# Kernel optimization log

Hardware: AMD Instinct MI355X
Metric: run time of the kernel (lower is better)

The kernel has to match this reference:

```python
import jax, jax.numpy as jnp
import numpy as np

C = 1024      # BIGNET_DIM
GROUPS = 256  # (1024*1024) / group_size(4096)

def _dequant(q4, norm):
    # q4: [GROUPS, 2048] ints in [0,256) packing two 4-bit codes per byte
    # (even positions = low nibble, odd positions = high nibble, as in
    #  block_quantize_4bit / block_dequantize_4bit). norm: [GROUPS, 1].
    lo = q4 % 16
    hi = q4 // 16
    q8 = jnp.stack([lo, hi], axis=-1).reshape(GROUPS, -1).astype(jnp.float32)  # [GROUPS, 4096]
    w = (q8 / 15.0 * 2.0 - 1.0) * norm
    return w.reshape(C, C)  # [out_features, in_features]

def setup_inputs() -> dict:
    key = jax.random.key(0)
    ks = jax.random.split(key, 6)
    x = jax.random.normal(ks[0], (16384, C), jnp.float32)
    wq4 = jax.random.randint(ks[1], (18, GROUPS, 2048), 0, 256, jnp.int32)
    wnorm = jax.random.uniform(ks[2], (18, GROUPS, 1), dtype=jnp.float32) * 0.05 + 1e-3
    lora_a = jax.random.normal(ks[3], (3, 32, C), jnp.float32) * 0.02
    lora_b = jax.random.normal(ks[4], (3, C, 32), jnp.float32) * 0.01
    ln_gamma = jnp.ones((5, C), jnp.float32)
    ln_beta = jnp.zeros((5, C), jnp.float32)
    return {"x": x, "wq4": wq4, "wnorm": wnorm, "lora_a": lora_a,
            "lora_b": lora_b, "ln_gamma": ln_gamma, "ln_beta": ln_beta}

def reference(x, wq4, wnorm, lora_a, lora_b, ln_gamma, ln_beta):
    def lin(h, i):
        # dequantize group-wise int4 weight, then linear (bias=False)
        return h @ _dequant(wq4[i], wnorm[i]).T

    def block(h, b, li):
        y = lin(h, 3 * b)
        if li is not None:  # QLoRALinear: parallel fp32 low-rank path
            y = y + (h @ lora_a[li].T) @ lora_b[li].T
        y = jax.nn.relu(y)
        y = jax.nn.relu(lin(y, 3 * b + 1))
        y = lin(y, 3 * b + 2)
        return y + h  # residual

    def ln(h, i):
        mu = jnp.mean(h, axis=-1, keepdims=True)
        var = jnp.mean((h - mu) ** 2, axis=-1, keepdims=True)
        return (h - mu) * jax.lax.rsqrt(var + 1e-5) * ln_gamma[i] + ln_beta[i]

    h = block(x, 0, 0); h = ln(h, 0)
    h = block(h, 1, None); h = ln(h, 1)
    h = block(h, 2, 1); h = ln(h, 2)
    h = block(h, 3, None); h = ln(h, 3)
    h = block(h, 4, 2); h = ln(h, 4)
    h = block(h, 5, None)
    return h
```

## Files before the change

### kernel.cpp

```cpp
#include <hip/hip_runtime.h>

typedef __bf16 bf16x8 __attribute__((ext_vector_type(8)));
typedef float f32x4 __attribute__((ext_vector_type(4)));

__device__ __forceinline__ unsigned short f32_to_bf16u(float f) {
  unsigned int u = __float_as_uint(f);
  u += 0x7fffu + ((u >> 16) & 1u);
  return (unsigned short)(u >> 16);
}
__device__ __forceinline__ float bf16u_to_f32(unsigned short s) {
  return __uint_as_float((unsigned int)s << 16);
}

__device__ __forceinline__ void async_copy16(const void* gptr, void* lptr) {
  __builtin_amdgcn_global_load_lds(
      (__attribute__((address_space(1))) void*)(unsigned long long)gptr,
      (__attribute__((address_space(3))) void*)(unsigned long long)lptr,
      16, 0, 0);
}

__global__ __launch_bounds__(256) void lora_ba_kernel(
    const float* __restrict__ lora_a, const float* __restrict__ lora_b,
    float* __restrict__ Wba)
{
  const int bid = blockIdx.x;
  const int li = bid >> 10;
  const int o = bid & 1023;
  const float* B = lora_b + li * 32768 + o * 32;
  const float* A = lora_a + li * 32768;
  const int c = threadIdx.x * 4;
  float4 acc = {0.f, 0.f, 0.f, 0.f};
#pragma unroll
  for (int r = 0; r < 32; r++) {
    const float br = B[r];
    const float4 a = *(const float4*)&A[r * 1024 + c];
    acc.x += br * a.x; acc.y += br * a.y; acc.z += br * a.z; acc.w += br * a.w;
  }
  *(float4*)&Wba[((size_t)li << 20) + o * 1024 + c] = acc;
}

__global__ __launch_bounds__(256) void dequant_kernel(
    const int* __restrict__ wq4, const float* __restrict__ wnorm,
    const float* __restrict__ Wba, unsigned short* __restrict__ Wd)
{
  const int gi = blockIdx.x * 256 + threadIdx.x;
  const int w = gi >> 19;
  const int rem = gi & 524287;
  const int q = wq4[gi];
  const float norm = wnorm[(w << 8) + (rem >> 11)];
  float w0 = ((float)(q & 15) * (2.0f / 15.0f) - 1.0f) * norm;
  float w1 = ((float)(q >> 4) * (2.0f / 15.0f) - 1.0f) * norm;
  const int p = rem << 1;
  const int li = (w == 0) ? 0 : (w == 6) ? 1 : (w == 12) ? 2 : -1;
  if (li >= 0) {
    const float2 ba = *(const float2*)&Wba[((size_t)li << 20) + p];
    w0 += ba.x;
    w1 += ba.y;
  }
  const unsigned int packed =
      ((unsigned int)f32_to_bf16u(w1) << 16) | (unsigned int)f32_to_bf16u(w0);
  *(unsigned int*)&Wd[((size_t)w << 20) + p] = packed;
}

__global__ __launch_bounds__(256) void cast_bf16_kernel(
    const float* __restrict__ x, unsigned short* __restrict__ o)
{
  const int i = blockIdx.x * 256 + threadIdx.x;
  const float4 v = ((const float4*)x)[i];
  ushort4 b;
  b.x = f32_to_bf16u(v.x);
  b.y = f32_to_bf16u(v.y);
  b.z = f32_to_bf16u(v.z);
  b.w = f32_to_bf16u(v.w);
  ((ushort4*)o)[i] = b;
}

template <int EPIL>
__global__ __launch_bounds__(512, 2) void gemm_bt(
    const unsigned short* __restrict__ A, const unsigned short* __restrict__ W,
    void* __restrict__ Out, const unsigned short* __restrict__ Res)
{
  constexpr int K = 1024;
  constexpr int N = 1024;
  __shared__ unsigned short lds[2][4][8192];

  const int tid = threadIdx.x;
  const int lane = tid & 63;
  const int wv = tid >> 6;
  const int wm = wv >> 2;
  const int wn = wv & 3;

  const int bid = blockIdx.x;
  const int l = (bid & 7) * 32 + (bid >> 3);
  const int m0 = (l >> 2) << 8;
  const int n0 = (l & 3) << 8;

  const int fr = lane & 15;
  const int q = lane >> 4;
  const int fr7 = fr & 7;

  const int srow = tid >> 3;
  const int schk = (tid & 7) ^ (srow & 7);
  const unsigned short* Asrc = A + (size_t)(m0 + srow) * K + schk * 8;
  const int nb0 = ((srow >> 5) << 6) + (srow & 31);
  const unsigned short* Wsrc = W + (size_t)(n0 + nb0) * K + schk * 8;

#define STAGE_A(mq, dbuf, kt)                                          \
  do {                                                                 \
    const unsigned short* s_ = Asrc + (size_t)(mq) * 64 * K + (kt);    \
    unsigned short* d_ = &lds[dbuf][(mq) ? 2 : 0][tid * 8];            \
    async_copy16(s_, d_);                                              \
    async_copy16(s_ + (size_t)128 * K, d_ + 4096);                     \
  } while (0)
#define STAGE_B(nq, dbuf, kt)                                          \
  do {                                                                 \
    const unsigned short* s_ = Wsrc + (size_t)(nq) * 32 * K + (kt);    \
    unsigned short* d_ = &lds[dbuf][(nq) ? 3 : 1][tid * 8];            \
    async_copy16(s_, d_);                                              \
    async_copy16(s_ + (size_t)128 * K, d_ + 4096);                     \
  } while (0)

  const int a_lane = (wm * 64 + fr) * 64;
  const int b_lane = (wn * 32 + fr) * 64;
  const int c0 = (q ^ fr7) << 3;
  const int c1 = ((4 + q) ^ fr7) << 3;

#define LDA4(dbuf, mq)                                                               \
  do {                                                                               \
    _Pragma("unroll") for (int ri = 0; ri < 4; ++ri) {                               \
      af[ri][0] = *(const bf16x8*)&lds[dbuf][(mq) ? 2 : 0][a_lane + ri * 1024 + c0]; \
      af[ri][1] = *(const bf16x8*)&lds[dbuf][(mq) ? 2 : 0][a_lane + ri * 1024 + c1]; \
    }                                                                                \
  } while (0)
#define LDB2(dst, dbuf, nq)                                                          \
  do {                                                                               \
    _Pragma("unroll") for (int rj = 0; rj < 2; ++rj) {                               \
      dst[rj][0] = *(const bf16x8*)&lds[dbuf][(nq) ? 3 : 1][b_lane + rj * 1024 + c0];\
      dst[rj][1] = *(const bf16x8*)&lds[dbuf][(nq) ? 3 : 1][b_lane + rj * 1024 + c1];\
    }                                                                                \
  } while (0)

#define MFMA16(ib, jb, BB)                                                    \
  do {                                                                        \
    __builtin_amdgcn_s_setprio(1);                                            \
    _Pragma("unroll") for (int i2 = 0; i2 < 4; ++i2)                          \
    _Pragma("unroll") for (int j2 = 0; j2 < 2; ++j2) {                        \
      acc[(ib) + i2][(jb) + j2] = __builtin_amdgcn_mfma_f32_16x16x32_bf16(    \
          af[i2][0], BB[j2][0], acc[(ib) + i2][(jb) + j2], 0, 0, 0);          \
      acc[(ib) + i2][(jb) + j2] = __builtin_amdgcn_mfma_f32_16x16x32_bf16(    \
          af[i2][1], BB[j2][1], acc[(ib) + i2][(jb) + j2], 0, 0, 0);          \
    }                                                                         \
    __builtin_amdgcn_s_setprio(0);                                            \
  } while (0)

#define OPEN_BAR  __builtin_amdgcn_s_barrier()
#define CLOSE_BAR asm volatile("s_barrier" ::: "memory")

  f32x4 acc[8][4];
#pragma unroll
  for (int a_ = 0; a_ < 8; ++a_)
#pragma unroll
    for (int b_ = 0; b_ < 4; ++b_) acc[a_][b_] = (f32x4){0.f, 0.f, 0.f, 0.f};

  bf16x8 af[4][2], bf0[2][2], bf1[2][2];

  STAGE_A(0, 0, 0);
  STAGE_B(0, 0, 0);
  STAGE_A(1, 0, 0);
  STAGE_B(1, 0, 0);
  STAGE_A(0, 1, 64);
  STAGE_B(0, 1, 64);
  STAGE_A(1, 1, 64);
  asm volatile("s_waitcnt vmcnt(6)" ::: "memory");
  __builtin_amdgcn_s_barrier();
  LDA4(0, 0);
  LDB2(bf0, 0, 0);

  for (int it = 0; it < K / 128; ++it) {
    const int kb = it * 128;
    const int k2 = (kb + 128 < K) ? (kb + 128) : (K - 64);
    const int k3 = (kb + 192 < K) ? (kb + 192) : (K - 64);

    LDB2(bf1, 0, 1);
    STAGE_B(1, 1, kb + 64);
    OPEN_BAR;
    MFMA16(0, 0, bf0);
    CLOSE_BAR;
    STAGE_A(0, 0, k2);
    OPEN_BAR;
    MFMA16(0, 2, bf1);
    LDA4(0, 1);
    CLOSE_BAR;
    STAGE_B(0, 0, k2);
    OPEN_BAR;
    MFMA16(4, 0, bf0);
    asm volatile("s_waitcnt vmcnt(4)" ::: "memory");
    CLOSE_BAR;
    LDB2(bf0, 1, 0);
    STAGE_A(1, 0, k2);
    OPEN_BAR;
    MFMA16(4, 2, bf1);
    LDA4(1, 0);
    CLOSE_BAR;
    LDB2(bf1, 1, 1);
    STAGE_B(1, 0, k2);
    OPEN_BAR;
    MFMA16(0, 0, bf0);
    CLOSE_BAR;
    STAGE_A(0, 1, k3);
    OPEN_BAR;
    MFMA16(0, 2, bf1);
    LDA4(1, 1);
    CLOSE_BAR;
    STAGE_B(0, 1, k3);
    OPEN_BAR;
    MFMA16(4, 0, bf0);
    asm volatile("s_waitcnt vmcnt(4)" ::: "memory");
    CLOSE_BAR;
    LDB2(bf0, 0, 0);
    STAGE_A(1, 1, k3);
    OPEN_BAR;
    MFMA16(4, 2, bf1);
    LDA4(0, 0);
    CLOSE_BAR;
  }

  const int mb = m0 + wm * 128 + q * 4;
  const int nb = n0 + wn * 64 + fr;
#pragma unroll
  for (int i2 = 0; i2 < 8; ++i2) {
#pragma unroll
    for (int r = 0; r < 4; ++r) {
      const int m = mb + i2 * 16 + r;
#pragma unroll
      for (int j2 = 0; j2 < 4; ++j2) {
        const int n = nb + j2 * 16;
        float v = acc[i2][j2][r];
        if (EPIL == 0) {
          v = v > 0.f ? v : 0.f;
          ((unsigned short*)Out)[(size_t)m * N + n] = f32_to_bf16u(v);
        } else if (EPIL == 1) {
          v += bf16u_to_f32(Res[(size_t)m * N + n]);
          ((unsigned short*)Out)[(size_t)m * N + n] = f32_to_bf16u(v);
        } else {
          v += bf16u_to_f32(Res[(size_t)m * N + n]);
          ((float*)Out)[(size_t)m * N + n] = v;
        }
      }
    }
  }
#undef STAGE_A
#undef STAGE_B
#undef LDA4
#undef LDB2
#undef MFMA16
#undef OPEN_BAR
#undef CLOSE_BAR
}

__global__ __launch_bounds__(256) void ln_kernel(
    const unsigned short* __restrict__ s_bf, const float* __restrict__ gamma,
    const float* __restrict__ beta, unsigned short* __restrict__ h_bf)
{
  const int row = blockIdx.x;
  const int tid = threadIdx.x;
  const size_t base = (size_t)row * 1024;
  const ushort4 u = ((const ushort4*)(s_bf + base))[tid];
  float v0 = bf16u_to_f32(u.x), v1 = bf16u_to_f32(u.y);
  float v2 = bf16u_to_f32(u.z), v3 = bf16u_to_f32(u.w);
  float s = v0 + v1 + v2 + v3;
  float s2 = v0 * v0 + v1 * v1 + v2 * v2 + v3 * v3;
#pragma unroll
  for (int off = 32; off > 0; off >>= 1) {
    s += __shfl_down(s, off, 64);
    s2 += __shfl_down(s2, off, 64);
  }
  __shared__ float red[8];
  if ((tid & 63) == 0) {
    red[tid >> 6] = s;
    red[4 + (tid >> 6)] = s2;
  }
  __syncthreads();
  s = red[0] + red[1] + red[2] + red[3];
  s2 = red[4] + red[5] + red[6] + red[7];
  const float mu = s * (1.0f / 1024.0f);
  const float var = s2 * (1.0f / 1024.0f) - mu * mu;
  const float rs = rsqrtf(var + 1e-5f);
  const float4 g = ((const float4*)gamma)[tid];
  const float4 bb = ((const float4*)beta)[tid];
  ushort4 ob;
  ob.x = f32_to_bf16u((v0 - mu) * rs * g.x + bb.x);
  ob.y = f32_to_bf16u((v1 - mu) * rs * g.y + bb.y);
  ob.z = f32_to_bf16u((v2 - mu) * rs * g.z + bb.z);
  ob.w = f32_to_bf16u((v3 - mu) * rs * g.w + bb.w);
  ((ushort4*)(h_bf + base))[tid] = ob;
}

extern "C" void kernel_launch(void* const* d_in, const int* in_sizes, int n_in,
                              void* d_out, int out_size, void* d_ws, size_t ws_size,
                              hipStream_t stream)
{
  const float* x = (const float*)d_in[0];
  const int* wq4 = (const int*)d_in[1];
  const float* wnorm = (const float*)d_in[2];
  const float* lora_a = (const float*)d_in[3];
  const float* lora_b = (const float*)d_in[4];
  const float* ln_g = (const float*)d_in[5];
  const float* ln_b = (const float*)d_in[6];
  float* out = (float*)d_out;

  char* ws = (char*)d_ws;
  unsigned short* Wd   = (unsigned short*)(ws);
  unsigned short* x_bf = (unsigned short*)(ws + 37748736);
  unsigned short* t1   = (unsigned short*)(ws + 71303168);
  unsigned short* t2   = (unsigned short*)(ws + 104857600);
  unsigned short* s_bf = (unsigned short*)(ws + 138412032);
  unsigned short* h_bf = (unsigned short*)(ws + 171966464);
  float* Wba           = (float*)(ws + 138412032);

  lora_ba_kernel<<<3072, 256, 0, stream>>>(lora_a, lora_b, Wba);
  dequant_kernel<<<36864, 256, 0, stream>>>(wq4, wnorm, Wba, Wd);
  cast_bf16_kernel<<<16384, 256, 0, stream>>>(x, x_bf);

  const unsigned short* hb = x_bf;
  const unsigned short* hres = x_bf;
  for (int b = 0; b < 6; b++) {
    const unsigned short* W0 = Wd + (size_t)(3 * b + 0) * 1048576;
    const unsigned short* W1 = Wd + (size_t)(3 * b + 1) * 1048576;
    const unsigned short* W2 = Wd + (size_t)(3 * b + 2) * 1048576;
    gemm_bt<0><<<256, 512, 0, stream>>>(hb, W0, t1, nullptr);
    gemm_bt<0><<<256, 512, 0, stream>>>(t1, W1, t2, nullptr);
    if (b < 5) {
      gemm_bt<1><<<256, 512, 0, stream>>>(t2, W2, s_bf, hres);
      ln_kernel<<<16384, 256, 0, stream>>>(s_bf, ln_g + b * 1024, ln_b + b * 1024, h_bf);
      hb = h_bf;
      hres = h_bf;
    } else {
      gemm_bt<2><<<256, 512, 0, stream>>>(t2, W2, out, hres);
    }
  }
  (void)in_sizes; (void)n_in; (void)out_size; (void)ws_size;
}
```

Measured before the change: 934.7 us.

## Stage bf16 GEMM epilogue through swizzled LDS for coalesced 16-byte stores

For the bf16-output GEMM epilogues (ReLU and residual), the accumulator tile is written into LDS using an XOR swizzle in two halves, then read back so each thread issues 16-byte global stores to contiguous row segments. This replaces the scattered 2-byte stores. The cast and layernorm kernels also remap block index to row, likely to spread consecutive blocks across XCDs for cache locality. The cost is extra barriers and LDS traffic in the epilogue, and the residual loads are still scattered 2-byte reads.

Result: slower. 1.018 ms (+8.9%).

```diff
diff --git a/kernel.cpp b/kernel.cpp
--- a/kernel.cpp
+++ b/kernel.cpp
@@ -65,7 +65,8 @@
 __global__ __launch_bounds__(256) void cast_bf16_kernel(
     const float* __restrict__ x, unsigned short* __restrict__ o)
 {
-  const int i = blockIdx.x * 256 + threadIdx.x;
+  const int row = ((blockIdx.x & 7) << 11) | (blockIdx.x >> 3);
+  const int i = row * 256 + threadIdx.x;
   const float4 v = ((const float4*)x)[i];
   ushort4 b;
   b.x = f32_to_bf16u(v.x);
@@ -225,28 +226,72 @@
     CLOSE_BAR;
   }
 
-  const int mb = m0 + wm * 128 + q * 4;
-  const int nb = n0 + wn * 64 + fr;
-#pragma unroll
-  for (int i2 = 0; i2 < 8; ++i2) {
-#pragma unroll
-    for (int r = 0; r < 4; ++r) {
-      const int m = mb + i2 * 16 + r;
-#pragma unroll
-      for (int j2 = 0; j2 < 4; ++j2) {
-        const int n = nb + j2 * 16;
-        float v = acc[i2][j2][r];
-        if (EPIL == 0) {
-          v = v > 0.f ? v : 0.f;
-          ((unsigned short*)Out)[(size_t)m * N + n] = f32_to_bf16u(v);
-        } else if (EPIL == 1) {
-          v += bf16u_to_f32(Res[(size_t)m * N + n]);
-          ((unsigned short*)Out)[(size_t)m * N + n] = f32_to_bf16u(v);
-        } else {
+  if (EPIL == 2) {
+    const int mb = m0 + wm * 128 + q * 4;
+    const int nb = n0 + wn * 64 + fr;
+#pragma unroll
+    for (int i2 = 0; i2 < 8; ++i2) {
+#pragma unroll
+      for (int r = 0; r < 4; ++r) {
+        const int m = mb + i2 * 16 + r;
+#pragma unroll
+        for (int j2 = 0; j2 < 4; ++j2) {
+          const int n = nb + j2 * 16;
+          float v = acc[i2][j2][r];
           v += bf16u_to_f32(Res[(size_t)m * N + n]);
           ((float*)Out)[(size_t)m * N + n] = v;
         }
       }
+    }
+  } else {
+    asm volatile("s_waitcnt vmcnt(0)" ::: "memory");
+    __syncthreads();
+    unsigned short* cs = (unsigned short*)&lds[0][0][0];
+#pragma unroll
+    for (int c = 0; c < 2; ++c) {
+      unsigned short resv[4][4][4];
+      if (EPIL == 1) {
+#pragma unroll
+        for (int i2p = 0; i2p < 4; ++i2p)
+#pragma unroll
+          for (int r = 0; r < 4; ++r)
+#pragma unroll
+            for (int j2 = 0; j2 < 4; ++j2) {
+              const int m = m0 + wm * 128 + (c * 4 + i2p) * 16 + q * 4 + r;
+              const int n = n0 + wn * 64 + j2 * 16 + fr;
+              resv[i2p][r][j2] = Res[(size_t)m * N + n];
+            }
+      }
+#pragma unroll
+      for (int i2p = 0; i2p < 4; ++i2p) {
+#pragma unroll
+        for (int r = 0; r < 4; ++r) {
+          const int lr = wm * 64 + i2p * 16 + q * 4 + r;
+#pragma unroll
+          for (int j2 = 0; j2 < 4; ++j2) {
+            float v = acc[c * 4 + i2p][j2][r];
+            if (EPIL == 0) v = v > 0.f ? v : 0.f;
+            else v += bf16u_to_f32(resv[i2p][r][j2]);
+            const int col = wn * 64 + j2 * 16 + fr;
+            const int sc = (col & 7) | ((((col >> 3) ^ (lr & 7)) & 31) << 3);
+            cs[lr * 256 + sc] = f32_to_bf16u(v);
+          }
+        }
+      }
+      __syncthreads();
+      {
+        const int lr = tid >> 2;
+        const int seg = tid & 3;
+        const int m = m0 + (lr >> 6) * 128 + c * 64 + (lr & 63);
+#pragma unroll
+        for (int jj = 0; jj < 8; ++jj) {
+          const int blk = (seg * 8 + jj) ^ (lr & 7);
+          const uint4 d = *(const uint4*)&cs[lr * 256 + blk * 8];
+          const int n = n0 + seg * 64 + jj * 8;
+          *(uint4*)&((unsigned short*)Out)[(size_t)m * N + n] = d;
+        }
+      }
+      __syncthreads();
     }
   }
 #undef STAGE_A
@@ -262,7 +307,7 @@
     const unsigned short* __restrict__ s_bf, const float* __restrict__ gamma,
     const float* __restrict__ beta, unsigned short* __restrict__ h_bf)
 {
-  const int row = blockIdx.x;
+  const int row = ((blockIdx.x & 7) << 11) | (blockIdx.x >> 3);
   const int tid = threadIdx.x;
   const size_t base = (size_t)row * 1024;
   const ushort4 u = ((const ushort4*)(s_bf + base))[tid];
```
